# Kernel tuning notes

Measured on AMD Instinct MI355X. Metric: run time of the kernel, lower is better.

Reference implementation:

```python
import jax, jax.numpy as jnp
import numpy as np
from jax import lax

B = 1024          # batch size (queries / docs)
H = 1536          # GRU hidden = embedding dim (hard-coded in module)
MAX_NEGS = 32     # max negatives per query
TEMP = 0.05       # opt.temperature


def setup_inputs() -> dict:
    key = jax.random.key(0)
    ks = jax.random.split(key, 8)
    rng = np.random.default_rng(0)
    lens = rng.integers(0, MAX_NEGS + 1, size=B)  # variable-length negs, some zero
    total = int(lens.sum())
    s = 0.02
    return {
        "q_emb": jax.random.normal(ks[0], (B, H), jnp.float32),
        "k_emb": jax.random.normal(ks[1], (B, H), jnp.float32),
        "inpn_emb": jax.random.normal(ks[2], (total, H), jnp.float32),
        "len_input_negs": jnp.asarray(lens, jnp.int32),
        "W_ih": jax.random.normal(ks[3], (3 * H, H), jnp.float32) * s,
        "W_hh": jax.random.normal(ks[4], (3 * H, H), jnp.float32) * s,
        "b_ih": jax.random.normal(ks[5], (3 * H,), jnp.float32) * s,
        "b_hh": jax.random.normal(ks[6], (3 * H,), jnp.float32) * s,
    }


def _ragged_gru_final(inpn_emb, lens, h0, W_ih, W_hh, b_ih, b_hh):
    """Batched equivalent of the per-sample torch GRU loop.

    For sample i: run a 1-layer GRU over inpn_emb[start_i:start_i+len_i]
    with initial hidden h0[i]; return final hidden (h0[i] if len_i == 0).
    """
    total = inpn_emb.shape[0]
    offsets = jnp.concatenate([jnp.zeros((1,), jnp.int32),
                               jnp.cumsum(lens)[:-1].astype(jnp.int32)])
    t = jnp.arange(MAX_NEGS, dtype=jnp.int32)
    idx = jnp.clip(offsets[:, None] + t[None, :], 0, total - 1)   # [B, Lmax]
    mask = t[None, :] < lens[:, None]                              # [B, Lmax]
    x_pad = inpn_emb[idx]                                          # [B, Lmax, H]

    def step(h, xm):
        x, m = xm                                  # x: [B,H], m: [B]
        gi = x @ W_ih.T + b_ih                     # [B, 3H]
        gh = h @ W_hh.T + b_hh                     # [B, 3H]
        i_r, i_z, i_n = jnp.split(gi, 3, axis=-1)
        h_r, h_z, h_n = jnp.split(gh, 3, axis=-1)
        r = jax.nn.sigmoid(i_r + h_r)
        z = jax.nn.sigmoid(i_z + h_z)
        n = jnp.tanh(i_n + r * h_n)
        h_new = (1.0 - z) * n + z * h
        h = jnp.where(m[:, None], h_new, h)        # freeze past end of seq
        return h, None

    h_final, _ = lax.scan(step, h0,
                          (x_pad.transpose(1, 0, 2), mask.T))
    return h_final


def reference(q_emb, k_emb, inpn_emb, len_input_negs, W_ih, W_hh, b_ih, b_hh):
    qemb = _ragged_gru_final(inpn_emb, len_input_negs, q_emb,
                             W_ih, W_hh, b_ih, b_hh)          # [B, H]
    scores = jnp.einsum("id,jd->ij", qemb / TEMP, k_emb)       # [B, B]
    labels = jnp.arange(B)
    logp = jax.nn.log_softmax(scores, axis=-1)
    loss = -jnp.mean(jnp.take_along_axis(logp, labels[:, None], axis=1))
    return loss
```

## Files before the change

kernel.cpp:

```cpp
#include <hip/hip_runtime.h>
#include <hip/hip_bf16.h>

#define B_SZ 1024
#define H_DIM 1536
#define H3 (3*H_DIM)
#define LMAX 32
#define TEMP_INV 20.0f

typedef __attribute__((ext_vector_type(4))) float f32x4;
typedef __attribute__((ext_vector_type(8))) short short8;
typedef unsigned short u16;
typedef unsigned int u32;

__device__ __forceinline__ u16 f2bf(float f){
  union { float f; u32 u; } v; v.f = f;
  u32 r = (v.u + 0x7FFFu + ((v.u >> 16) & 1u)) >> 16;
  return (u16)r;
}
__device__ __forceinline__ u32 pack2(float lo, float hi){
  return (u32)f2bf(lo) | ((u32)f2bf(hi) << 16);
}
__device__ __forceinline__ float bf2f(u16 b){
  union { u32 u; float f; } v; v.u = ((u32)b) << 16; return v.f;
}
__device__ __forceinline__ float sigm(float x){ return 1.f / (1.f + __expf(-x)); }

__device__ __forceinline__ void gload_lds16(const void* g, void* l){
  __builtin_amdgcn_global_load_lds(
      (const __attribute__((address_space(1))) void*)g,
      (__attribute__((address_space(3))) void*)l, 16, 0, 0);
}

__global__ void sort_kernel(const int* __restrict__ lens, int* __restrict__ rank,
                            int* __restrict__ cnt_arr, int* __restrict__ tstart,
                            int* __restrict__ rowmap)
{
  __shared__ int wavecnt[33][17];
  __shared__ int bintot[33];
  __shared__ int scnt[LMAX];
  __shared__ int sts[LMAX];
  __shared__ int soff[B_SZ];
  int i = threadIdx.x;
  int li = lens[i];
  int w = i >> 6, lane = i & 63;

  if (i < 33 * 17) ((int*)wavecnt)[i] = 0;
  __syncthreads();

  int mypre = 0;
  #pragma unroll 1
  for (int b = 0; b <= 32; ++b) {
    unsigned long long m = __ballot(li == b);
    if (lane == 0) wavecnt[b][w] = __popcll(m);
    if (b == li) mypre = __popcll(m & ((1ull << lane) - 1ull));
  }
  __syncthreads();

  if (i < 33) {
    int c = 0;
    #pragma unroll 1
    for (int w2 = 0; w2 < 16; ++w2) c += wavecnt[i][w2];
    bintot[i] = c;
  }
  __syncthreads();

  int wpre = 0;
  #pragma unroll 1
  for (int w2 = 0; w2 < w; ++w2) wpre += wavecnt[li][w2];
  int base = 0;
  #pragma unroll 1
  for (int b = li + 1; b <= 32; ++b) base += bintot[b];
  int r = base + wpre + mypre;
  rank[i] = r;

  if (i < LMAX) {
    int c = 0;
    #pragma unroll 1
    for (int b = i + 1; b <= 32; ++b) c += bintot[b];
    scnt[i] = c; cnt_arr[i] = c;
  }
  __syncthreads();
  if (i == 0) {
    int acc = 0;
    for (int t = 0; t < LMAX; ++t) { sts[t] = acc; tstart[t] = acc; acc += scnt[t]; }
  }

  soff[i] = li;
  __syncthreads();
  for (int off = 1; off < B_SZ; off <<= 1) {
    int v = (i >= off) ? soff[i - off] : 0;
    __syncthreads();
    soff[i] += v;
    __syncthreads();
  }
  int myoff = soff[i] - li;
  for (int t = 0; t < li; ++t)
    rowmap[myoff + t] = sts[t] + r;
}

__global__ void prep_kernel(const float* __restrict__ wih, const float* __restrict__ whh,
                            const float* __restrict__ kemb, const float* __restrict__ qemb,
                            const int* __restrict__ rank,
                            u16* __restrict__ wih_bf, u16* __restrict__ whh_bf,
                            u16* __restrict__ k_bf, u16* __restrict__ h0)
{
  size_t o = ((size_t)blockIdx.x * 256 + threadIdx.x) * 8;
  if (o < (size_t)H3 * H_DIM) {
    float4 a0 = *(const float4*)(wih + o), a1 = *(const float4*)(wih + o + 4);
    *(uint4*)(wih_bf + o) = make_uint4(pack2(a0.x,a0.y), pack2(a0.z,a0.w),
                                       pack2(a1.x,a1.y), pack2(a1.z,a1.w));
    float4 b0 = *(const float4*)(whh + o), b1 = *(const float4*)(whh + o + 4);
    *(uint4*)(whh_bf + o) = make_uint4(pack2(b0.x,b0.y), pack2(b0.z,b0.w),
                                       pack2(b1.x,b1.y), pack2(b1.z,b1.w));
  }
  if (o < (size_t)B_SZ * H_DIM) {
    float4 k0 = *(const float4*)(kemb + o), k1 = *(const float4*)(kemb + o + 4);
    *(uint4*)(k_bf + o) = make_uint4(pack2(k0.x,k0.y), pack2(k0.z,k0.w),
                                     pack2(k1.x,k1.y), pack2(k1.z,k1.w));
    int i = (int)(o / H_DIM), col = (int)(o % H_DIM);
    float4 q0 = *(const float4*)(qemb + o), q1 = *(const float4*)(qemb + o + 4);
    *(uint4*)(h0 + (size_t)rank[i] * H_DIM + col) =
        make_uint4(pack2(q0.x,q0.y), pack2(q0.z,q0.w),
                   pack2(q1.x,q1.y), pack2(q1.z,q1.w));
  }
}

__global__ void convx_kernel(const float* __restrict__ x, const int* __restrict__ rowmap,
                             u16* __restrict__ xt, int total){
  size_t o = ((size_t)blockIdx.x * 256 + threadIdx.x) * 8;
  int row = (int)(o / H_DIM), col = (int)(o % H_DIM);
  if (row < total) {
    float4 a0 = *(const float4*)(x + o), a1 = *(const float4*)(x + o + 4);
    *(uint4*)(xt + (size_t)rowmap[row] * H_DIM + col) =
        make_uint4(pack2(a0.x,a0.y), pack2(a0.z,a0.w),
                   pack2(a1.x,a1.y), pack2(a1.z,a1.w));
  } else {
    *(uint4*)(xt + o) = make_uint4(0,0,0,0);
  }
}

__global__ __launch_bounds__(256, 2) void gi_gemm_kernel(
    const u16* __restrict__ x_bf, const u16* __restrict__ wih_bf,
    const float* __restrict__ b_ih, u16* __restrict__ gi, int nblk_m)
{
  int nblk = nblk_m * 36;
  int id = blockIdx.x;
  int q8 = nblk >> 3, r8 = nblk & 7;
  int xcd = id & 7, off = id >> 3;
  int swz = (xcd < r8) ? (xcd * (q8 + 1) + off) : (r8 * (q8 + 1) + (xcd - r8) * q8 + off);
  int bx = swz / 36, by = swz % 36;

  __shared__ u16 lds[2 * 128 * 64];
  char* ldsb = (char*)lds;
  int tid = threadIdx.x, wid = tid >> 6, lane = tid & 63;
  int wm = wid >> 1, wn = wid & 1;
  int lrow = lane & 15, lkh = lane >> 4;
  f32x4 acc[4][4] = {};

  for (int kt = 0; kt < 24; ++kt) {
    int k0 = kt * 64;
    #pragma unroll
    for (int it = 0; it < 8; ++it) {
      int cb = it * 256 + wid * 64;
      int c  = cb + lane;
      int isB = c >> 10;
      int cc  = c & 1023;
      int row = cc >> 3, slot = cc & 7;
      const u16* src = isB ? (wih_bf + (size_t)(by * 128 + row) * H_DIM)
                           : (x_bf  + (size_t)(bx * 128 + row) * H_DIM);
      src += k0 + ((slot ^ (row & 7)) << 3);
      gload_lds16(src, ldsb + (size_t)cb * 16);
    }
    __syncthreads();
    #pragma unroll
    for (int qq = 0; qq < 2; ++qq) {
      short8 a[4], b[4];
      int slot = qq * 4 + lkh;
      #pragma unroll
      for (int m = 0; m < 4; ++m) {
        int row = wm * 64 + m * 16 + lrow;
        a[m] = *(const short8*)(ldsb + row * 128 + ((slot ^ (row & 7)) << 4));
      }
      #pragma unroll
      for (int n = 0; n < 4; ++n) {
        int row = wn * 64 + n * 16 + lrow;
        b[n] = *(const short8*)(ldsb + 16384 + row * 128 + ((slot ^ (row & 7)) << 4));
      }
      #pragma unroll
      for (int m = 0; m < 4; ++m)
        #pragma unroll
        for (int n = 0; n < 4; ++n)
          acc[m][n] = __builtin_amdgcn_mfma_f32_16x16x32_bf16(a[m], b[n], acc[m][n], 0,0,0);
    }
    __syncthreads();
  }
  #pragma unroll
  for (int n = 0; n < 4; ++n) {
    int j = by * 128 + wn * 64 + n * 16 + lrow;
    float bias = b_ih[j];
    #pragma unroll
    for (int m = 0; m < 4; ++m)
      #pragma unroll
      for (int r4 = 0; r4 < 4; ++r4) {
        int rowg = bx * 128 + wm * 64 + m * 16 + lkh * 4 + r4;
        gi[(size_t)rowg * 4608 + j] = f2bf(acc[m][n][r4] + bias);
      }
  }
}

__global__ __launch_bounds__(512, 4) void gh_step_kernel(
    const u16* __restrict__ h_cur, u16* __restrict__ h_nxt,
    const u16* __restrict__ whh_bf, const u16* __restrict__ gi,
    const float* __restrict__ b_hh,
    const int* __restrict__ cnt_arr, const int* __restrict__ tstart, int t)
{
  int cnt = cnt_arr[t];
  int bid = blockIdx.x;
  int x8 = bid & 7, jj = bid >> 3;
  int ct = x8 * 3 + jj % 3;
  int bx = jj / 3;
  if (bx * 64 >= cnt) return;
  int ts = tstart[t];

  __shared__ u16 lds[2 * 16384];
  char* ldsb = (char*)lds;

  int tid = threadIdx.x, wid = tid >> 6, lane = tid & 63;
  int wm = wid >> 2, wn = wid & 3;
  int lrow = lane & 15, lkh = lane >> 4;
  f32x4 acc[3][2] = {};
  float hold[2][4];

  auto STAGE = [&](int buf, int kt){
    int k0 = kt * 64;
    char* base = ldsb + buf * 32768;
    #pragma unroll
    for (int it = 0; it < 4; ++it) {
      int cb = it * 512 + wid * 64;
      int c  = cb + lane;
      const u16* src;
      if (c < 512) {
        int row = c >> 3, slot = c & 7;
        int ridx = bx * 64 + row; if (ridx >= cnt) ridx = cnt - 1;
        src = h_cur + (size_t)ridx * H_DIM + k0 + ((slot ^ (row & 7)) << 3);
      } else {
        int w = c - 512;
        int slab = w >> 9, row = (w >> 3) & 63, slot = w & 7;
        src = whh_bf + (size_t)(slab * H_DIM + ct * 64 + row) * H_DIM
              + k0 + ((slot ^ (row & 7)) << 3);
      }
      gload_lds16(src, base + (size_t)cb * 16);
    }
  };

  auto COMPUTE = [&](int buf){
    char* base = ldsb + buf * 32768;
    #pragma unroll
    for (int qq = 0; qq < 2; ++qq) {
      short8 ah[2], bw[3];
      int slot = qq * 4 + lkh;
      #pragma unroll
      for (int m = 0; m < 2; ++m) {
        int row = wm * 32 + m * 16 + lrow;
        ah[m] = *(const short8*)(base + row * 128 + ((slot ^ (row & 7)) << 4));
      }
      {
        int row = wn * 16 + lrow;
        int byte = row * 128 + ((slot ^ (row & 7)) << 4);
        #pragma unroll
        for (int s = 0; s < 3; ++s)
          bw[s] = *(const short8*)(base + 8192 + s * 8192 + byte);
      }
      #pragma unroll
      for (int s = 0; s < 3; ++s)
        #pragma unroll
        for (int m = 0; m < 2; ++m)
          acc[s][m] = __builtin_amdgcn_mfma_f32_16x16x32_bf16(
              ah[m], bw[s], acc[s][m], 0, 0, 0);
    }
  };

  STAGE(0, 0);
  for (int kt = 0; kt < 24; ++kt) {
    if (kt + 1 < 24) {
      STAGE((kt + 1) & 1, kt + 1);
      asm volatile("s_waitcnt vmcnt(4)" ::: "memory");
    } else {
      asm volatile("s_waitcnt vmcnt(0)" ::: "memory");
    }
    __builtin_amdgcn_sched_barrier(0);
    __builtin_amdgcn_s_barrier();
    __builtin_amdgcn_sched_barrier(0);
    COMPUTE(kt & 1);
    if (kt == ct) {
      char* base = ldsb + (kt & 1) * 32768;
      int col = wn * 16 + lrow;
      int slot = col >> 3, within = col & 7;
      #pragma unroll
      for (int m = 0; m < 2; ++m)
        #pragma unroll
        for (int r4 = 0; r4 < 4; ++r4) {
          int row = wm * 32 + m * 16 + lkh * 4 + r4;
          hold[m][r4] = bf2f(*(const u16*)(base + row * 128 +
                             ((slot ^ (row & 7)) << 4) + within * 2));
        }
    }
    __builtin_amdgcn_s_barrier();
    __builtin_amdgcn_sched_barrier(0);
  }

  {
    int lc = wn * 16 + lrow;
    int j = ct * 64 + lc;
    float bhr = b_hh[j], bhz = b_hh[H_DIM + j], bhn = b_hh[2*H_DIM + j];
    #pragma unroll
    for (int m = 0; m < 2; ++m)
      #pragma unroll
      for (int r4 = 0; r4 < 4; ++r4) {
        int lm = wm * 32 + m * 16 + lkh * 4 + r4;
        int ridx = bx * 64 + lm;
        if (ridx < cnt) {
          size_t gr = (size_t)(ts + ridx) * 4608;
          float gir = bf2f(__builtin_nontemporal_load(&gi[gr + j]));
          float giz = bf2f(__builtin_nontemporal_load(&gi[gr + H_DIM + j]));
          float gin = bf2f(__builtin_nontemporal_load(&gi[gr + 2*H_DIM + j]));
          float rr = sigm(gir + acc[0][m][r4] + bhr);
          float zz = sigm(giz + acc[1][m][r4] + bhz);
          float nn = tanhf(gin + rr * (acc[2][m][r4] + bhn));
          h_nxt[(size_t)ridx * H_DIM + j] = f2bf((1.f - zz) * nn + zz * hold[m][r4]);
        }
      }
  }
}

__global__ __launch_bounds__(256, 2) void scores_kernel(
    const u16* __restrict__ h0, const u16* __restrict__ h1,
    const int* __restrict__ lens, const int* __restrict__ rank,
    const u16* __restrict__ k_bf, float* __restrict__ scores)
{
  int bx = blockIdx.x, by = blockIdx.y;
  __shared__ u16 lds[2 * 64 * 64];
  char* ldsb = (char*)lds;
  int tid = threadIdx.x, wid = tid >> 6, lane = tid & 63;
  int wm = wid >> 1, wn = wid & 1;
  int lrow = lane & 15, lkh = lane >> 4;
  f32x4 acc[2][2] = {};

  for (int kt = 0; kt < 24; ++kt) {
    int k0 = kt * 64;
    #pragma unroll
    for (int it = 0; it < 4; ++it) {
      int cb = it * 256 + wid * 64;
      int c  = cb + lane;
      int isB = c >> 9;
      int cc  = c & 511;
      int row = cc >> 3, slot = cc & 7;
      const u16* src;
      if (!isB) {
        int g = bx * 64 + row;
        src = ((lens[g] & 1) ? h1 : h0) + (size_t)rank[g] * H_DIM;
      } else {
        src = k_bf + (size_t)(by * 64 + row) * H_DIM;
      }
      src += k0 + ((slot ^ (row & 7)) << 3);
      gload_lds16(src, ldsb + (size_t)cb * 16);
    }
    __syncthreads();
    #pragma unroll
    for (int qq = 0; qq < 2; ++qq) {
      short8 a[2], b[2];
      int slot = qq * 4 + lkh;
      #pragma unroll
      for (int m = 0; m < 2; ++m) {
        int row = wm * 32 + m * 16 + lrow;
        a[m] = *(const short8*)(ldsb + row * 128 + ((slot ^ (row & 7)) << 4));
      }
      #pragma unroll
      for (int n = 0; n < 2; ++n) {
        int row = wn * 32 + n * 16 + lrow;
        b[n] = *(const short8*)(ldsb + 8192 + row * 128 + ((slot ^ (row & 7)) << 4));
      }
      #pragma unroll
      for (int m = 0; m < 2; ++m)
        #pragma unroll
        for (int n = 0; n < 2; ++n)
          acc[m][n] = __builtin_amdgcn_mfma_f32_16x16x32_bf16(a[m], b[n], acc[m][n], 0,0,0);
    }
    __syncthreads();
  }
  #pragma unroll
  for (int m = 0; m < 2; ++m)
    #pragma unroll
    for (int n = 0; n < 2; ++n) {
      int col = by * 64 + wn * 32 + n * 16 + lrow;
      #pragma unroll
      for (int r4 = 0; r4 < 4; ++r4) {
        int rowg = bx * 64 + wm * 32 + m * 16 + lkh * 4 + r4;
        scores[(size_t)rowg * B_SZ + col] = acc[m][n][r4] * TEMP_INV;
      }
    }
}

__global__ void softmax_kernel(const float* __restrict__ scores, float* __restrict__ row_loss){
  int i = blockIdx.x;
  int tid = threadIdx.x;
  const float* row = scores + (size_t)i * B_SZ;
  __shared__ float red[4];
  float m = -INFINITY;
  for (int j = tid; j < B_SZ; j += 256) m = fmaxf(m, row[j]);
  for (int off = 32; off; off >>= 1) m = fmaxf(m, __shfl_xor(m, off));
  if ((tid & 63) == 0) red[tid >> 6] = m;
  __syncthreads();
  m = fmaxf(fmaxf(red[0], red[1]), fmaxf(red[2], red[3]));
  __syncthreads();
  float s = 0.f;
  for (int j = tid; j < B_SZ; j += 256) s += __expf(row[j] - m);
  for (int off = 32; off; off >>= 1) s += __shfl_xor(s, off);
  if ((tid & 63) == 0) red[tid >> 6] = s;
  __syncthreads();
  if (tid == 0) {
    float S = red[0] + red[1] + red[2] + red[3];
    row_loss[i] = m + __logf(S) - row[i];
  }
}

__global__ void final_kernel(const float* __restrict__ row_loss, float* __restrict__ out){
  __shared__ float s[B_SZ];
  int i = threadIdx.x;
  s[i] = row_loss[i]; __syncthreads();
  for (int off = 512; off; off >>= 1) {
    if (i < off) s[i] += s[i + off];
    __syncthreads();
  }
  if (i == 0) out[0] = s[0] * (1.0f / B_SZ);
}

extern "C" void kernel_launch(void* const* d_in, const int* in_sizes, int n_in,
                              void* d_out, int out_size, void* d_ws, size_t ws_size,
                              hipStream_t stream) {
  const float* q_emb = (const float*)d_in[0];
  const float* k_emb = (const float*)d_in[1];
  const float* inpn  = (const float*)d_in[2];
  const int*   lens  = (const int*)d_in[3];
  const float* wih   = (const float*)d_in[4];
  const float* whh   = (const float*)d_in[5];
  const float* bih   = (const float*)d_in[6];
  const float* bhh   = (const float*)d_in[7];
  float* out = (float*)d_out;

  int total  = in_sizes[2] / H_DIM;
  int mtiles = (total + 127) / 128;
  int Mpad   = mtiles * 128;

  char* p = (char*)d_ws;
  auto alloc = [&](size_t bytes){ char* r = p; p += (bytes + 255) & ~(size_t)255; return r; };
  int* rank      = (int*)alloc(B_SZ * 4);
  int* cnt_arr   = (int*)alloc(LMAX * 4);
  int* tstart    = (int*)alloc(LMAX * 4);
  int* rowmap    = (int*)alloc((size_t)Mpad * 4);
  u16* hbuf0     = (u16*)alloc((size_t)B_SZ * H_DIM * 2);
  u16* hbuf1     = (u16*)alloc((size_t)B_SZ * H_DIM * 2);
  u16* wih_bf    = (u16*)alloc((size_t)H3 * H_DIM * 2);
  u16* whh_bf    = (u16*)alloc((size_t)H3 * H_DIM * 2);
  u16* k_bf      = (u16*)alloc((size_t)B_SZ * H_DIM * 2);
  u16* xt        = (u16*)alloc((size_t)Mpad * H_DIM * 2);
  u16* gi        = (u16*)alloc((size_t)Mpad * H3 * 2);
  float* scores  = (float*)alloc((size_t)B_SZ * B_SZ * 4);
  float* row_loss= (float*)alloc(B_SZ * 4);
  if ((size_t)(p - (char*)d_ws) > ws_size) return;

  sort_kernel<<<1, B_SZ, 0, stream>>>(lens, rank, cnt_arr, tstart, rowmap);
  prep_kernel<<<(H3 * H_DIM / 8) / 256, 256, 0, stream>>>(
      wih, whh, k_emb, q_emb, rank, wih_bf, whh_bf, k_bf, hbuf0);
  convx_kernel<<<((size_t)Mpad * H_DIM / 8) / 256, 256, 0, stream>>>(
      inpn, rowmap, xt, total);

  gi_gemm_kernel<<<mtiles * 36, 256, 0, stream>>>(xt, wih_bf, bih, gi, mtiles);

  for (int t = 0; t < LMAX; ++t) {
    u16* hc = (t & 1) ? hbuf1 : hbuf0;
    u16* hn = (t & 1) ? hbuf0 : hbuf1;
    gh_step_kernel<<<384, 512, 0, stream>>>(
        hc, hn, whh_bf, gi, bhh, cnt_arr, tstart, t);
  }

  scores_kernel<<<dim3(B_SZ / 64, B_SZ / 64), 256, 0, stream>>>(
      hbuf0, hbuf1, lens, rank, k_bf, scores);
  softmax_kernel<<<B_SZ, 256, 0, stream>>>(scores, row_loss);
  final_kernel<<<1, B_SZ, 0, stream>>>(row_loss, out);
}
```

Before: 1.112 ms.

## Enlarge gi GEMM tile to 256x256 with double-buffered LDS pipeline

Rewrites the input-gate GEMM to use 256x256 output tiles with 512 threads and a two-stage LDS double buffer. Global-to-LDS loads for tile k+2 are issued while MFMAs run on the current tile, and explicit waitcnt, barriers and setprio control the interleaving. This aims to raise arithmetic intensity and hide global load latency. It uses 128KB of LDS per block, which lowers occupancy, and padding M to 256 adds wasted rows.

```diff
diff --git a/kernel.cpp b/kernel.cpp
--- a/kernel.cpp
+++ b/kernel.cpp
@@ -139,71 +139,119 @@
   }
 }
 
-__global__ __launch_bounds__(256, 2) void gi_gemm_kernel(
+__global__ __launch_bounds__(512, 2) void gi_gemm_kernel(
     const u16* __restrict__ x_bf, const u16* __restrict__ wih_bf,
-    const float* __restrict__ b_ih, u16* __restrict__ gi, int nblk_m)
+    const float* __restrict__ b_ih, u16* __restrict__ gi, int mt)
 {
-  int nblk = nblk_m * 36;
+  int nblk = mt * 18;
   int id = blockIdx.x;
   int q8 = nblk >> 3, r8 = nblk & 7;
   int xcd = id & 7, off = id >> 3;
   int swz = (xcd < r8) ? (xcd * (q8 + 1) + off) : (r8 * (q8 + 1) + (xcd - r8) * q8 + off);
-  int bx = swz / 36, by = swz % 36;
-
-  __shared__ u16 lds[2 * 128 * 64];
+  int bx = swz / 18, by = swz % 18;
+
+  __shared__ u16 lds[2 * 32768];
   char* ldsb = (char*)lds;
+
   int tid = threadIdx.x, wid = tid >> 6, lane = tid & 63;
-  int wm = wid >> 1, wn = wid & 1;
+  int wm = wid >> 2, wn = wid & 3;
   int lrow = lane & 15, lkh = lane >> 4;
-  f32x4 acc[4][4] = {};
-
+
+  f32x4 acc[8][4] = {};
+
+  auto STAGE = [&](int buf, int kt){
+    int k0 = kt * 64;
+    char* base = ldsb + buf * 65536;
+    #pragma unroll
+    for (int it = 0; it < 8; ++it) {
+      int cb = it * 512 + wid * 64;
+      int c  = cb + lane;
+      int isB = c >> 11;
+      int cc  = c & 2047;
+      int row = cc >> 3, slot = cc & 7;
+      const u16* src = isB ? (wih_bf + (size_t)(by * 256 + row) * H_DIM)
+                           : (x_bf  + (size_t)(bx * 256 + row) * H_DIM);
+      src += k0 + ((slot ^ (row & 7)) << 3);
+      gload_lds16(src, base + (size_t)cb * 16);
+    }
+  };
+
+  STAGE(0, 0);
+  STAGE(1, 1);
   for (int kt = 0; kt < 24; ++kt) {
-    int k0 = kt * 64;
-    #pragma unroll
-    for (int it = 0; it < 8; ++it) {
-      int cb = it * 256 + wid * 64;
-      int c  = cb + lane;
-      int isB = c >> 10;
-      int cc  = c & 1023;
-      int row = cc >> 3, slot = cc & 7;
-      const u16* src = isB ? (wih_bf + (size_t)(by * 128 + row) * H_DIM)
-                           : (x_bf  + (size_t)(bx * 128 + row) * H_DIM);
-      src += k0 + ((slot ^ (row & 7)) << 3);
-      gload_lds16(src, ldsb + (size_t)cb * 16);
-    }
-    __syncthreads();
-    #pragma unroll
-    for (int qq = 0; qq < 2; ++qq) {
-      short8 a[4], b[4];
-      int slot = qq * 4 + lkh;
-      #pragma unroll
-      for (int m = 0; m < 4; ++m) {
-        int row = wm * 64 + m * 16 + lrow;
-        a[m] = *(const short8*)(ldsb + row * 128 + ((slot ^ (row & 7)) << 4));
-      }
-      #pragma unroll
-      for (int n = 0; n < 4; ++n) {
-        int row = wn * 64 + n * 16 + lrow;
-        b[n] = *(const short8*)(ldsb + 16384 + row * 128 + ((slot ^ (row & 7)) << 4));
-      }
-      #pragma unroll
-      for (int m = 0; m < 4; ++m)
+    int b = kt & 1;
+    char* abase = ldsb + b * 65536;
+    char* bbase = abase + 32768;
+    if (kt < 23) asm volatile("s_waitcnt vmcnt(8)" ::: "memory");
+    else         asm volatile("s_waitcnt vmcnt(0)" ::: "memory");
+    __builtin_amdgcn_sched_barrier(0);
+    __builtin_amdgcn_s_barrier();
+    __builtin_amdgcn_sched_barrier(0);
+
+    short8 bfr[4][2], afr[4][2];
+    #pragma unroll
+    for (int cf = 0; cf < 4; ++cf)
+      #pragma unroll
+      for (int ks = 0; ks < 2; ++ks) {
+        int row = wn * 64 + cf * 16 + lrow;
+        int slot = ks * 4 + lkh;
+        bfr[cf][ks] = *(const short8*)(bbase + row * 128 + ((slot ^ (row & 7)) << 4));
+      }
+    #pragma unroll
+    for (int rf = 0; rf < 4; ++rf)
+      #pragma unroll
+      for (int ks = 0; ks < 2; ++ks) {
+        int row = wm * 128 + rf * 16 + lrow;
+        int slot = ks * 4 + lkh;
+        afr[rf][ks] = *(const short8*)(abase + row * 128 + ((slot ^ (row & 7)) << 4));
+      }
+    asm volatile("s_waitcnt lgkmcnt(0)" ::: "memory");
+    __builtin_amdgcn_sched_barrier(0);
+    __builtin_amdgcn_s_setprio(1);
+    #pragma unroll
+    for (int rf = 0; rf < 4; ++rf)
+      #pragma unroll
+      for (int cf = 0; cf < 4; ++cf)
         #pragma unroll
-        for (int n = 0; n < 4; ++n)
-          acc[m][n] = __builtin_amdgcn_mfma_f32_16x16x32_bf16(a[m], b[n], acc[m][n], 0,0,0);
-    }
-    __syncthreads();
-  }
+        for (int ks = 0; ks < 2; ++ks)
+          acc[rf][cf] = __builtin_amdgcn_mfma_f32_16x16x32_bf16(
+              afr[rf][ks], bfr[cf][ks], acc[rf][cf], 0, 0, 0);
+    __builtin_amdgcn_s_setprio(0);
+    #pragma unroll
+    for (int rf = 0; rf < 4; ++rf)
+      #pragma unroll
+      for (int ks = 0; ks < 2; ++ks) {
+        int row = wm * 128 + (4 + rf) * 16 + lrow;
+        int slot = ks * 4 + lkh;
+        afr[rf][ks] = *(const short8*)(abase + row * 128 + ((slot ^ (row & 7)) << 4));
+      }
+    asm volatile("s_waitcnt lgkmcnt(0)" ::: "memory");
+    __builtin_amdgcn_sched_barrier(0);
+    __builtin_amdgcn_s_barrier();
+    __builtin_amdgcn_sched_barrier(0);
+    if (kt + 2 < 24) STAGE(b, kt + 2);
+    __builtin_amdgcn_s_setprio(1);
+    #pragma unroll
+    for (int rf = 0; rf < 4; ++rf)
+      #pragma unroll
+      for (int cf = 0; cf < 4; ++cf)
+        #pragma unroll
+        for (int ks = 0; ks < 2; ++ks)
+          acc[4 + rf][cf] = __builtin_amdgcn_mfma_f32_16x16x32_bf16(
+              afr[rf][ks], bfr[cf][ks], acc[4 + rf][cf], 0, 0, 0);
+    __builtin_amdgcn_s_setprio(0);
+  }
+
   #pragma unroll
-  for (int n = 0; n < 4; ++n) {
-    int j = by * 128 + wn * 64 + n * 16 + lrow;
+  for (int cf = 0; cf < 4; ++cf) {
+    int j = by * 256 + wn * 64 + cf * 16 + lrow;
     float bias = b_ih[j];
     #pragma unroll
-    for (int m = 0; m < 4; ++m)
+    for (int rf = 0; rf < 8; ++rf)
       #pragma unroll
       for (int r4 = 0; r4 < 4; ++r4) {
-        int rowg = bx * 128 + wm * 64 + m * 16 + lkh * 4 + r4;
-        gi[(size_t)rowg * 4608 + j] = f2bf(acc[m][n][r4] + bias);
+        int rowg = bx * 256 + wm * 128 + rf * 16 + lkh * 4 + r4;
+        gi[(size_t)rowg * 4608 + j] = f2bf(acc[rf][cf][r4] + bias);
       }
   }
 }
@@ -449,8 +497,8 @@
   float* out = (float*)d_out;
 
   int total  = in_sizes[2] / H_DIM;
-  int mtiles = (total + 127) / 128;
-  int Mpad   = mtiles * 128;
+  int mtiles = (total + 255) / 256;
+  int Mpad   = mtiles * 256;
 
   char* p = (char*)d_ws;
   auto alloc = [&](size_t bytes){ char* r = p; p += (bytes + 255) & ~(size_t)255; return r; };
@@ -475,7 +523,7 @@
   convx_kernel<<<((size_t)Mpad * H_DIM / 8) / 256, 256, 0, stream>>>(
       inpn, rowmap, xt, total);
 
-  gi_gemm_kernel<<<mtiles * 36, 256, 0, stream>>>(xt, wih_bf, bih, gi, mtiles);
+  gi_gemm_kernel<<<mtiles * 18, 512, 0, stream>>>(xt, wih_bf, bih, gi, mtiles);
 
   for (int t = 0; t < LMAX; ++t) {
     u16* hc = (t & 1) ? hbuf1 : hbuf0;
```

Measured after the change: 1.072 ms. 1.04x faster.
